# Optimization experiments

Measured on AMD Instinct MI355X. Metric: run time of the kernel, lower is better.

## Reference

```python
import jax, jax.numpy as jnp
import numpy as np

B, A, T = 256, 512, 21
DIM = 128
SC = 6
NHEAD, HD = 4, DIM // 4

def conv1d_relu(x, w, b, stride=2):
    # x: (N, C, L), w: (O, I, K)
    y = jax.lax.conv_general_dilated(x, w, (stride,), 'SAME', dimension_numbers=('NCH', 'OIH', 'NCH'))
    return jax.nn.relu(y + b[None, :, None])

def to_vector(feat, vm):
    vec_mask = vm[..., :-1] & vm[..., 1:]
    while vec_mask.ndim < feat.ndim:
        vec_mask = vec_mask[..., None]
    return jnp.where(vec_mask, feat[:, :, 1:] - feat[:, :, :-1], jnp.zeros_like(feat[:, :, 1:]))

def setup_inputs():
    key = jax.random.key(0)
    ks = jax.random.split(key, 24)
    f32 = jnp.float32
    inp = {}
    inp['position'] = jax.random.normal(ks[0], (B, A, T, 2), f32)
    inp['heading'] = jax.random.normal(ks[1], (B, A, T), f32)
    inp['velocity'] = jax.random.normal(ks[2], (B, A, T, 2), f32)
    inp['shape'] = jax.random.uniform(ks[3], (B, A, T, 2), f32)
    inp['current_state'] = jax.random.normal(ks[4], (B, SC), f32)
    inp['category'] = jax.random.randint(ks[5], (B, A), 0, 4)
    inp['valid_mask'] = jax.random.randint(ks[6], (B, A, T), 0, 2).astype(bool)
    # history encoder (CNN) params: 9 -> 32 -> 64 -> 128 channels, k=3, stride 2
    inp['conv1_w'] = jax.random.normal(ks[7], (32, 9, 3), f32) * 0.1
    inp['conv1_b'] = jnp.zeros((32,), f32)
    inp['conv2_w'] = jax.random.normal(ks[8], (64, 32, 3), f32) * 0.1
    inp['conv2_b'] = jnp.zeros((64,), f32)
    inp['conv3_w'] = jax.random.normal(ks[9], (128, 64, 3), f32) * 0.1
    inp['conv3_b'] = jnp.zeros((128,), f32)
    # StateAttentionEncoder params
    inp['se_w'] = jax.random.normal(ks[10], (SC, DIM), f32) * 0.02   # per-channel Linear(1,dim) weights
    inp['se_b'] = jnp.zeros((SC, DIM), f32)
    inp['pos_embed'] = jax.random.normal(ks[11], (1, SC, DIM), f32) * 0.02
    inp['query'] = jax.random.normal(ks[12], (1, 1, DIM), f32) * 0.02
    inp['in_proj_w'] = jax.random.normal(ks[13], (3 * DIM, DIM), f32) * (1.0 / np.sqrt(DIM))
    inp['in_proj_b'] = jnp.zeros((3 * DIM,), f32)
    inp['out_proj_w'] = jax.random.normal(ks[14], (DIM, DIM), f32) * (1.0 / np.sqrt(DIM))
    inp['out_proj_b'] = jnp.zeros((DIM,), f32)
    inp['type_emb'] = jax.random.normal(ks[15], (4, DIM), f32) * 0.02
    return inp

def reference(position, heading, velocity, shape, current_state, category, valid_mask,
              conv1_w, conv1_b, conv2_w, conv2_b, conv3_w, conv3_b,
              se_w, se_b, pos_embed, query, in_proj_w, in_proj_b, out_proj_w, out_proj_b,
              type_emb):
    # --- build per-step agent features (B, A, T-1, 9) ---
    heading_vec = to_vector(heading, valid_mask)
    valid_mask_vec = valid_mask[..., 1:] & valid_mask[..., :-1]
    agent_feature = jnp.concatenate([
        to_vector(position, valid_mask),
        to_vector(velocity, valid_mask),
        jnp.stack([jnp.cos(heading_vec), jnp.sin(heading_vec)], axis=-1),
        shape[:, :, 1:],
        valid_mask_vec.astype(jnp.float32)[..., None],
    ], axis=-1)
    bs, nA, Tm1, C = agent_feature.shape
    x = agent_feature.reshape(bs * nA, Tm1, C).transpose(0, 2, 1)  # (N, 9, T-1)
    # --- history CNN encoder (applied to all rows, then masked; same math as boolean gather/scatter) ---
    h = conv1d_relu(x, conv1_w, conv1_b)
    h = conv1d_relu(h, conv2_w, conv2_b)
    h = conv1d_relu(h, conv3_w, conv3_b)
    enc = h.mean(axis=-1)  # (N, DIM)
    valid_agent = valid_mask.any(-1).reshape(-1)
    x_agent = jnp.where(valid_agent[:, None], enc, 0.0).reshape(bs, nA, DIM)
    # --- ego state attention encoder (eval mode: no token dropout) ---
    ego = current_state[:, :SC]
    x_embed = ego[:, :, None] * se_w[None] + se_b[None] + pos_embed  # (B, SC, DIM)
    Wq, Wk, Wv = in_proj_w[:DIM], in_proj_w[DIM:2 * DIM], in_proj_w[2 * DIM:]
    bq, bk, bv = in_proj_b[:DIM], in_proj_b[DIM:2 * DIM], in_proj_b[2 * DIM:]
    q = (query[0, 0] @ Wq.T + bq).reshape(NHEAD, HD)             # (H, D)
    k = (x_embed @ Wk.T + bk).reshape(bs, SC, NHEAD, HD)          # (B, S, H, D)
    v = (x_embed @ Wv.T + bv).reshape(bs, SC, NHEAD, HD)
    scores = jnp.einsum('hd,bshd->bhs', q, k) * (1.0 / np.sqrt(HD))
    attn = jax.nn.softmax(scores, axis=-1)
    o = jnp.einsum('bhs,bshd->bhd', attn, v).reshape(bs, DIM)
    x_ego = o @ out_proj_w.T + out_proj_b                         # (B, DIM)
    x_agent = x_agent.at[:, 0].set(x_ego)
    # --- type embedding add ---
    return x_agent + type_emb[category]
```

## Files before the change

kernel.cpp:

```cpp
#include <hip/hip_runtime.h>
#include <hip/hip_bf16.h>


#define BB 256
#define AAG 512
#define TT 21
#define NAG (BB * AAG)

typedef __hip_bfloat16 bf16;
typedef __attribute__((ext_vector_type(8))) short s8v;
typedef __attribute__((ext_vector_type(4))) float f4v;

__device__ int g_dtype;
__device__ int g_mask_mode;
__device__ __align__(16) short g_w1p[32 * 64];
__device__ __align__(16) short g_w2p[64 * 96];
__device__ __align__(16) short g_w3p[128 * 192];
__device__ __align__(16) float g_b1[32];
__device__ __align__(16) float g_b2[64];
__device__ __align__(16) float g_b3[128];

template <int DT>
__device__ __forceinline__ float ldf(const void* p, long i) {
    if (DT) return __bfloat162float(((const bf16*)p)[i]);
    return ((const float*)p)[i];
}
template <int DT>
__device__ __forceinline__ void stf(void* p, long i, float v) {
    if (DT) ((bf16*)p)[i] = __float2bfloat16(v);
    else    ((float*)p)[i] = v;
}
__device__ __forceinline__ unsigned short f2bu(float x) {
    bf16 b = __float2bfloat16(x);
    union { bf16 b; unsigned short u; } cv; cv.b = b; return cv.u;
}
__device__ __forceinline__ float bu2f(unsigned short u) {
    union { unsigned int i; float f; } cv; cv.i = ((unsigned int)u) << 16; return cv.f;
}
template <int DT>
__device__ __forceinline__ float2 ldf2(const void* p, long i) {
    if (DT) {
        unsigned int u = *(const unsigned int*)((const bf16*)p + i);
        return make_float2(bu2f((unsigned short)(u & 0xffffu)),
                           bu2f((unsigned short)(u >> 16)));
    }
    return *(const float2*)((const float*)p + i);
}
__device__ __forceinline__ bool mask_at(const void* p, long i, int mode) {
    if (mode == 0) return ((const int*)p)[i] != 0;
    if (mode == 1) return ((const unsigned char*)p)[i] != 0;
    if (mode == 2) return ((const float*)p)[i] != 0.f;
    return (((const unsigned short*)p)[i] & 0x7fff) != 0;
}

__global__ void detect_kernel(const unsigned int* __restrict__ pw,
                              const unsigned char* __restrict__ m) {
    __shared__ int cls[4];
    __shared__ int mv;
    __shared__ int good;
    int tid = threadIdx.x;
    if (tid < 4) cls[tid] = 0;
    if (tid == 0) { mv = 0; good = 0; }
    __syncthreads();
    int g = 0;
    for (int i = tid; i < 1024; i += 256) {
        unsigned int w = pw[i];
        unsigned int h0 = w & 0xffffu, h1 = w >> 16;
        unsigned int e0 = (h0 >> 7) & 0xff, e1 = (h1 >> 7) & 0xff;
        if (h0 == 0 || (e0 >= 90 && e0 <= 160)) g++;
        if (h1 == 0 || (e1 >= 90 && e1 <= 160)) g++;
    }
    atomicAdd(&good, g);
    int l0 = 0, l1 = 0, l2 = 0, l3 = 0, lm = 0;
    for (int i = tid; i < 4096; i += 256) {
        int v = m[i];
        if (v) {
            switch (i & 3) { case 0: l0 = 1; break; case 1: l1 = 1; break;
                             case 2: l2 = 1; break; default: l3 = 1; }
            if (v > lm) lm = v;
        }
    }
    if (l0) atomicOr(&cls[0], 1);
    if (l1) atomicOr(&cls[1], 1);
    if (l2) atomicOr(&cls[2], 1);
    if (l3) atomicOr(&cls[3], 1);
    atomicMax(&mv, lm);
    __syncthreads();
    if (tid == 0) {
        g_dtype = (good >= 1740) ? 1 : 0;
        int mode;
        if (!cls[1] && !cls[2] && !cls[3]) mode = 0;
        else if (!cls[0] && !cls[1])       mode = 2;
        else if (mv <= 1)                  mode = 1;
        else                               mode = 3;
        g_mask_mode = mode;
    }
}

template <int DT>
__global__ void prep_weights_kernel(const void* __restrict__ w1, const void* __restrict__ b1,
                                    const void* __restrict__ w2, const void* __restrict__ b2,
                                    const void* __restrict__ w3, const void* __restrict__ b3) {
    if (g_dtype != DT) return;
    int tid = blockIdx.x * blockDim.x + threadIdx.x;
    int nt = gridDim.x * blockDim.x;
    for (int i = tid; i < 32 * 64; i += nt) {
        int oc = i >> 6, k = i & 63, tap = k >> 4, ic = k & 15;
        float v = (tap < 3 && ic < 9) ? ldf<DT>(w1, oc * 27 + ic * 3 + tap) : 0.f;
        g_w1p[i] = (short)f2bu(v);
    }
    for (int i = tid; i < 64 * 96; i += nt) {
        int oc = i / 96, k = i % 96, tap = k >> 5, ic = k & 31;
        g_w2p[i] = (short)f2bu(ldf<DT>(w2, oc * 96 + ic * 3 + tap));
    }
    for (int i = tid; i < 128 * 192; i += nt) {
        int oc = i / 192, k = i % 192, tap = k >> 6, ic = k & 63;
        g_w3p[i] = (short)f2bu(ldf<DT>(w3, oc * 192 + ic * 3 + tap));
    }
    for (int i = tid; i < 32; i += nt) g_b1[i] = ldf<DT>(b1, i);
    for (int i = tid; i < 64; i += nt) g_b2[i] = ldf<DT>(b2, i);
    for (int i = tid; i < 128; i += nt) g_b3[i] = ldf<DT>(b3, i);
}

#define FEAT_RS 24
#define FEAT_AS 568
#define H1_RS 40
#define H1_AS 440
#define H2_RS 72
#define H2_AS 504
#define C3_AS 392
#define OFF_H1 9088
#define OFF_VALID 32256
#define SMEM_BYTES 32320

#define MFMA16(a, b, c) __builtin_amdgcn_mfma_f32_16x16x32_bf16((a), (b), (c), 0, 0, 0)

template <int DT>
__global__ __launch_bounds__(256) void stage1_kernel(
    const void* __restrict__ pos, const void* __restrict__ heading,
    const void* __restrict__ vel, const void* __restrict__ shp,
    const void* __restrict__ vmask, const int* __restrict__ category,
    const void* __restrict__ type_emb, void* __restrict__ out) {
    if (g_dtype != DT) return;
    __shared__ __align__(16) char smem[SMEM_BYTES];
    short* feat = (short*)smem;
    short* h1   = (short*)smem + OFF_H1;
    short* h2   = (short*)smem;
    short* c3   = (short*)smem + OFF_H1;
    int* s_valid = (int*)(smem + OFF_VALID);

    const int tid = threadIdx.x;
    const int wave = tid >> 6, lane = tid & 63;
    const int col = lane & 15, quad = lane >> 4;
    const long agent0 = (long)blockIdx.x * 16;
    const int mode = g_mask_mode;

    if (tid < 16) s_valid[tid] = 0;
    {
        unsigned int* h1u = (unsigned int*)h1;
        h1u[(tid >> 4) * 220 + 200 + (tid & 15)] = 0;
    }
    __syncthreads();

    for (int idx = tid; idx < 16 * 22; idx += 256) {
        int ag = idx / 22, t = idx % 22;
        short* row = feat + ag * FEAT_AS + t * FEAT_RS;
        if (t >= 20) {
            *(uint4*)row = make_uint4(0, 0, 0, 0);
            *(uint4*)(row + 8) = make_uint4(0, 0, 0, 0);
            if (t == 20) {
                long base = (agent0 + ag) * TT + 20;
                if (mask_at(vmask, base, mode)) atomicOr(&s_valid[ag], 1);
            }
        } else {
            long base = (agent0 + ag) * TT + t;
            bool vmt = mask_at(vmask, base, mode);
            if (vmt) atomicOr(&s_valid[ag], 1);
            bool m2 = vmt && mask_at(vmask, base + 1, mode);
            float2 pa = ldf2<DT>(pos, base * 2), pb = ldf2<DT>(pos, base * 2 + 2);
            float2 va = ldf2<DT>(vel, base * 2), vb = ldf2<DT>(vel, base * 2 + 2);
            float hh0 = ldf<DT>(heading, base), hh1 = ldf<DT>(heading, base + 1);
            float2 sv = ldf2<DT>(shp, base * 2 + 2);
            float dh = m2 ? (hh1 - hh0) : 0.f;
            float sn, cn;
            __sincosf(dh, &sn, &cn);
            unsigned int p0 = f2bu(m2 ? pb.x - pa.x : 0.f) | ((unsigned int)f2bu(m2 ? pb.y - pa.y : 0.f) << 16);
            unsigned int p1 = f2bu(m2 ? vb.x - va.x : 0.f) | ((unsigned int)f2bu(m2 ? vb.y - va.y : 0.f) << 16);
            unsigned int p2 = f2bu(cn) | ((unsigned int)f2bu(sn) << 16);
            unsigned int p3 = f2bu(sv.x) | ((unsigned int)f2bu(sv.y) << 16);
            unsigned int p4 = (unsigned int)f2bu(m2 ? 1.f : 0.f);
            *(uint4*)row = make_uint4(p0, p1, p2, p3);
            *(uint4*)(row + 8) = make_uint4(p4, 0, 0, 0);
        }
    }
    __syncthreads();

    {
        int Mt = wave >> 1;
        int oc = Mt * 16 + col;
        s8v a0 = *(const s8v*)(g_w1p + oc * 64 + quad * 8);
        s8v a1 = *(const s8v*)(g_w1p + oc * 64 + 32 + quad * 8);
        int k0 = quad * 8, k1 = 32 + quad * 8;
        int tap0 = k0 >> 4, ic0 = k0 & 15;
        int tap1 = k1 >> 4, ic1 = k1 & 15;
        int ocr = Mt * 16 + quad * 4;
        f4v bia = *(const f4v*)(g_b1 + ocr);
        int ag = col;
        const short* agbase = feat + ag * FEAT_AS;
#pragma unroll
        for (int i = 0; i < 5; i++) {
            int p = (wave & 1) * 5 + i;
            const short* bb = agbase + 2 * p * FEAT_RS;
            s8v b0 = *(const s8v*)(bb + tap0 * FEAT_RS + ic0);
            s8v b1 = *(const s8v*)(bb + tap1 * FEAT_RS + ic1);
            f4v acc = {0.f, 0.f, 0.f, 0.f};
            acc = MFMA16(a0, b0, acc);
            acc = MFMA16(a1, b1, acc);
            unsigned int lo = f2bu(fmaxf(acc[0] + bia[0], 0.f)) | ((unsigned int)f2bu(fmaxf(acc[1] + bia[1], 0.f)) << 16);
            unsigned int hi = f2bu(fmaxf(acc[2] + bia[2], 0.f)) | ((unsigned int)f2bu(fmaxf(acc[3] + bia[3], 0.f)) << 16);
            *(uint2*)(h1 + ag * H1_AS + p * H1_RS + ocr) = make_uint2(lo, hi);
        }
    }
    __syncthreads();

    {
        unsigned int* h2u = (unsigned int*)h2;
        for (int i = tid; i < 1024; i += 256) {
            int a2 = i >> 6, r = (i >> 5) & 1, cc = i & 31;
            h2u[a2 * 252 + r * 216 + cc] = 0;
        }
        int Mt = wave;
        int oc = Mt * 16 + col;
        s8v a[3];
#pragma unroll
        for (int ks = 0; ks < 3; ks++)
            a[ks] = *(const s8v*)(g_w2p + oc * 96 + ks * 32 + quad * 8);
        int ocr = Mt * 16 + quad * 4;
        f4v bia = *(const f4v*)(g_b2 + ocr);
        int ag = col;
#pragma unroll
        for (int p = 0; p < 5; p++) {
            f4v acc = {0.f, 0.f, 0.f, 0.f};
#pragma unroll
            for (int ks = 0; ks < 3; ks++) {
                s8v b = *(const s8v*)(h1 + ag * H1_AS + (2 * p + ks) * H1_RS + quad * 8);
                acc = MFMA16(a[ks], b, acc);
            }
            unsigned int lo = f2bu(fmaxf(acc[0] + bia[0], 0.f)) | ((unsigned int)f2bu(fmaxf(acc[1] + bia[1], 0.f)) << 16);
            unsigned int hi = f2bu(fmaxf(acc[2] + bia[2], 0.f)) | ((unsigned int)f2bu(fmaxf(acc[3] + bia[3], 0.f)) << 16);
            *(uint2*)(h2 + ag * H2_AS + (p + 1) * H2_RS + ocr) = make_uint2(lo, hi);
        }
    }
    __syncthreads();

#pragma unroll
    for (int m2 = 0; m2 < 2; m2++) {
        int Mt = wave * 2 + m2;
        int oc = Mt * 16 + col;
        s8v a[6];
#pragma unroll
        for (int ks = 0; ks < 6; ks++)
            a[ks] = *(const s8v*)(g_w3p + oc * 192 + ks * 32 + quad * 8);
        int ocr = Mt * 16 + quad * 4;
        f4v bia = *(const f4v*)(g_b3 + ocr);
        int ag = col;
#pragma unroll
        for (int p = 0; p < 3; p++) {
            f4v acc = {0.f, 0.f, 0.f, 0.f};
#pragma unroll
            for (int ks = 0; ks < 6; ks++) {
                int kg = ks * 32 + quad * 8;
                int tap = kg >> 6, ic = kg & 63;
                s8v b = *(const s8v*)(h2 + ag * H2_AS + (2 * p + tap) * H2_RS + ic);
                acc = MFMA16(a[ks], b, acc);
            }
            unsigned int lo = f2bu(fmaxf(acc[0] + bia[0], 0.f)) | ((unsigned int)f2bu(fmaxf(acc[1] + bia[1], 0.f)) << 16);
            unsigned int hi = f2bu(fmaxf(acc[2] + bia[2], 0.f)) | ((unsigned int)f2bu(fmaxf(acc[3] + bia[3], 0.f)) << 16);
            *(uint2*)(c3 + ag * C3_AS + p * 128 + ocr) = make_uint2(lo, hi);
        }
    }
    __syncthreads();

    {
        int ag = tid >> 4;
        int ocg = (tid & 15) * 8;
        const short* cb = c3 + ag * C3_AS;
        s8v x0 = *(const s8v*)(cb + ocg);
        s8v x1 = *(const s8v*)(cb + 128 + ocg);
        s8v x2 = *(const s8v*)(cb + 256 + ocg);
        int valid = s_valid[ag];
        long agl = agent0 + ag;
        int cat = category[agl];
        float vals[8];
#pragma unroll
        for (int j = 0; j < 8; j++) {
            float m = (bu2f((unsigned short)x0[j]) + bu2f((unsigned short)x1[j]) +
                       bu2f((unsigned short)x2[j])) * (1.f / 3.f);
            vals[j] = valid ? m : 0.f;
        }
        if (DT) {
            s8v te = *(const s8v*)((const bf16*)type_emb + (long)cat * 128 + ocg);
            s8v o;
#pragma unroll
            for (int j = 0; j < 8; j++)
                o[j] = (short)f2bu(vals[j] + bu2f((unsigned short)te[j]));
            *(s8v*)((bf16*)out + agl * 128 + ocg) = o;
        } else {
            const float4* tep = (const float4*)((const float*)type_emb + (long)cat * 128 + ocg);
            float4 t0 = tep[0], t1 = tep[1];
            float4 o0 = make_float4(vals[0] + t0.x, vals[1] + t0.y, vals[2] + t0.z, vals[3] + t0.w);
            float4 o1 = make_float4(vals[4] + t1.x, vals[5] + t1.y, vals[6] + t1.z, vals[7] + t1.w);
            float4* op = (float4*)((float*)out + agl * 128 + ocg);
            op[0] = o0; op[1] = o1;
        }
    }
}

template <int DT>
__global__ __launch_bounds__(128) void stage2_kernel(
    const void* __restrict__ cs, const int* __restrict__ category,
    const void* __restrict__ se_w, const void* __restrict__ se_b,
    const void* __restrict__ pe, const void* __restrict__ query,
    const void* __restrict__ ipw, const void* __restrict__ ipb,
    const void* __restrict__ opw, const void* __restrict__ opb,
    const void* __restrict__ type_emb, void* __restrict__ out) {
    if (g_dtype != DT) return;
    int b = blockIdx.x, d = threadIdx.x;
    __shared__ float s_xe[6][128];
    __shared__ float s_qu[128];
    __shared__ float s_q[128];
    __shared__ float s_k[6][128];
    __shared__ float s_v[6][128];
    __shared__ float s_att[4][6];
    __shared__ float s_o[128];

    s_qu[d] = ldf<DT>(query, d);
#pragma unroll
    for (int s = 0; s < 6; s++) {
        float ego = ldf<DT>(cs, b * 6 + s);
        s_xe[s][d] = fmaf(ego, ldf<DT>(se_w, s * 128 + d),
                          ldf<DT>(se_b, s * 128 + d) + ldf<DT>(pe, s * 128 + d));
    }
    __syncthreads();

    float accq = ldf<DT>(ipb, d);
    float bk = ldf<DT>(ipb, 128 + d), bv = ldf<DT>(ipb, 256 + d);
    float acck[6], accv[6];
#pragma unroll
    for (int s = 0; s < 6; s++) { acck[s] = bk; accv[s] = bv; }
    for (int e = 0; e < 128; e++) {
        float wqe = ldf<DT>(ipw, (long)d * 128 + e);
        accq = fmaf(s_qu[e], wqe, accq);
        float wke = ldf<DT>(ipw, (long)(128 + d) * 128 + e);
        float wve = ldf<DT>(ipw, (long)(256 + d) * 128 + e);
#pragma unroll
        for (int s = 0; s < 6; s++) {
            float xe = s_xe[s][e];
            acck[s] = fmaf(xe, wke, acck[s]);
            accv[s] = fmaf(xe, wve, accv[s]);
        }
    }
    s_q[d] = accq;
#pragma unroll
    for (int s = 0; s < 6; s++) { s_k[s][d] = acck[s]; s_v[s][d] = accv[s]; }
    __syncthreads();

    if (d < 4) {
        float sc[6];
        float mx = -1e30f;
#pragma unroll
        for (int s = 0; s < 6; s++) {
            float t = 0.f;
            for (int q = 0; q < 32; q++) t = fmaf(s_q[d * 32 + q], s_k[s][d * 32 + q], t);
            t *= 0.17677669529663687f;
            sc[s] = t;
            mx = fmaxf(mx, t);
        }
        float sum = 0.f;
#pragma unroll
        for (int s = 0; s < 6; s++) { sc[s] = expf(sc[s] - mx); sum += sc[s]; }
        float inv = 1.f / sum;
#pragma unroll
        for (int s = 0; s < 6; s++) s_att[d][s] = sc[s] * inv;
    }
    __syncthreads();

    {
        int h = d >> 5;
        float o = 0.f;
#pragma unroll
        for (int s = 0; s < 6; s++) o = fmaf(s_att[h][s], s_v[s][d], o);
        s_o[d] = o;
    }
    __syncthreads();

    float acc = ldf<DT>(opb, d);
    for (int e = 0; e < 128; e++) acc = fmaf(s_o[e], ldf<DT>(opw, (long)d * 128 + e), acc);
    int cat = category[(long)b * AAG];
    stf<DT>(out, (long)b * AAG * 128 + d, acc + ldf<DT>(type_emb, cat * 128 + d));
}

extern "C" void kernel_launch(void* const* d_in, const int* in_sizes, int n_in,
                              void* d_out, int out_size, void* d_ws, size_t ws_size,
                              hipStream_t stream) {
    const void* position      = d_in[0];
    const void* heading       = d_in[1];
    const void* velocity      = d_in[2];
    const void* shape         = d_in[3];
    const void* current_state = d_in[4];
    const int*  category      = (const int*)d_in[5];
    const void* valid_mask    = d_in[6];
    const void* conv1_w = d_in[7];
    const void* conv1_b = d_in[8];
    const void* conv2_w = d_in[9];
    const void* conv2_b = d_in[10];
    const void* conv3_w = d_in[11];
    const void* conv3_b = d_in[12];
    const void* se_w    = d_in[13];
    const void* se_b    = d_in[14];
    const void* pos_embed = d_in[15];
    const void* query     = d_in[16];
    const void* in_proj_w = d_in[17];
    const void* in_proj_b = d_in[18];
    const void* out_proj_w = d_in[19];
    const void* out_proj_b = d_in[20];
    const void* type_emb   = d_in[21];

    hipLaunchKernelGGL(detect_kernel, dim3(1), dim3(256), 0, stream,
                       (const unsigned int*)position, (const unsigned char*)valid_mask);

    hipLaunchKernelGGL(prep_weights_kernel<0>, dim3(64), dim3(256), 0, stream,
                       conv1_w, conv1_b, conv2_w, conv2_b, conv3_w, conv3_b);
    hipLaunchKernelGGL(prep_weights_kernel<1>, dim3(64), dim3(256), 0, stream,
                       conv1_w, conv1_b, conv2_w, conv2_b, conv3_w, conv3_b);

    hipLaunchKernelGGL(stage1_kernel<0>, dim3(NAG / 16), dim3(256), 0, stream,
                       position, heading, velocity, shape, valid_mask, category, type_emb, d_out);
    hipLaunchKernelGGL(stage1_kernel<1>, dim3(NAG / 16), dim3(256), 0, stream,
                       position, heading, velocity, shape, valid_mask, category, type_emb, d_out);

    hipLaunchKernelGGL(stage2_kernel<0>, dim3(BB), dim3(128), 0, stream,
                       current_state, category, se_w, se_b, pos_embed, query,
                       in_proj_w, in_proj_b, out_proj_w, out_proj_b, type_emb, d_out);
    hipLaunchKernelGGL(stage2_kernel<1>, dim3(BB), dim3(128), 0, stream,
                       current_state, category, se_w, se_b, pos_embed, query,
                       in_proj_w, in_proj_b, out_proj_w, out_proj_b, type_emb, d_out);
}
```

Baseline: 304.5 us.

## Fuse launches into prep and combined kernels; fold query into key weights

Merges the dtype detection and weight-prep kernels into one prep kernel, which also precomputes the query projected through Wk (per-head vectors plus bias) so attention scores need only a dot with the embedded state. Stage1 and stage2 are fused into a single launch with a runtime dtype branch, replacing the separate launches per dtype. Stage2 applies attention before the V projection and splits the row dot products across 256 threads. Stage1 skips writing the agent-0 rows that stage2 overwrites, removing the write-write ordering dependence. Each block in the prep kernel redoes the detection scan, and the fused kernel carries code for both stages and both dtypes, which may raise register use.

```diff
diff --git a/kernel.cpp b/kernel.cpp
--- a/kernel.cpp
+++ b/kernel.cpp
@@ -19,6 +19,8 @@
 __device__ __align__(16) float g_b1[32];
 __device__ __align__(16) float g_b2[64];
 __device__ __align__(16) float g_b3[128];
+__device__ __align__(16) float g_wqk[4 * 128];
+__device__ __align__(16) float g_qb[4];
 
 template <int DT>
 __device__ __forceinline__ float ldf(const void* p, long i) {
@@ -53,11 +55,100 @@
     return (((const unsigned short*)p)[i] & 0x7fff) != 0;
 }
 
-__global__ void detect_kernel(const unsigned int* __restrict__ pw,
-                              const unsigned char* __restrict__ m) {
+template <int DT>
+__device__ __forceinline__ float rowdot64(const void* W, long off, const float* y) {
+    float acc = 0.f;
+    if (DT) {
+        const unsigned short* wr = (const unsigned short*)W + off;
+#pragma unroll
+        for (int i = 0; i < 8; i++) {
+            uint4 w = *(const uint4*)(wr + i * 8);
+            acc = fmaf(bu2f((unsigned short)(w.x & 0xffffu)), y[i * 8 + 0], acc);
+            acc = fmaf(bu2f((unsigned short)(w.x >> 16)),     y[i * 8 + 1], acc);
+            acc = fmaf(bu2f((unsigned short)(w.y & 0xffffu)), y[i * 8 + 2], acc);
+            acc = fmaf(bu2f((unsigned short)(w.y >> 16)),     y[i * 8 + 3], acc);
+            acc = fmaf(bu2f((unsigned short)(w.z & 0xffffu)), y[i * 8 + 4], acc);
+            acc = fmaf(bu2f((unsigned short)(w.z >> 16)),     y[i * 8 + 5], acc);
+            acc = fmaf(bu2f((unsigned short)(w.w & 0xffffu)), y[i * 8 + 6], acc);
+            acc = fmaf(bu2f((unsigned short)(w.w >> 16)),     y[i * 8 + 7], acc);
+        }
+    } else {
+        const float* wr = (const float*)W + off;
+#pragma unroll
+        for (int i = 0; i < 16; i++) {
+            float4 w = *(const float4*)(wr + i * 4);
+            acc = fmaf(w.x, y[i * 4 + 0], acc);
+            acc = fmaf(w.y, y[i * 4 + 1], acc);
+            acc = fmaf(w.z, y[i * 4 + 2], acc);
+            acc = fmaf(w.w, y[i * 4 + 3], acc);
+        }
+    }
+    return acc;
+}
+
+template <int DT>
+__device__ __forceinline__ void prep_body(const void* w1, const void* b1,
+                                          const void* w2, const void* b2,
+                                          const void* w3, const void* b3) {
+    int tid = blockIdx.x * 256 + threadIdx.x;
+    const int nt = 64 * 256;
+    for (int i = tid; i < 32 * 64; i += nt) {
+        int oc = i >> 6, k = i & 63, tap = k >> 4, ic = k & 15;
+        float v = (tap < 3 && ic < 9) ? ldf<DT>(w1, oc * 27 + ic * 3 + tap) : 0.f;
+        g_w1p[i] = (short)f2bu(v);
+    }
+    for (int i = tid; i < 64 * 96; i += nt) {
+        int oc = i / 96, k = i % 96, tap = k >> 5, ic = k & 31;
+        g_w2p[i] = (short)f2bu(ldf<DT>(w2, oc * 96 + ic * 3 + tap));
+    }
+    for (int i = tid; i < 128 * 192; i += nt) {
+        int oc = i / 192, k = i % 192, tap = k >> 6, ic = k & 63;
+        g_w3p[i] = (short)f2bu(ldf<DT>(w3, oc * 192 + ic * 3 + tap));
+    }
+    for (int i = tid; i < 32; i += nt) g_b1[i] = ldf<DT>(b1, i);
+    for (int i = tid; i < 64; i += nt) g_b2[i] = ldf<DT>(b2, i);
+    for (int i = tid; i < 128; i += nt) g_b3[i] = ldf<DT>(b3, i);
+}
+
+template <int DT>
+__device__ __forceinline__ void qprep_body(const void* query, const void* ipw,
+                                           const void* ipb, float* sq) {
+    int tid = threadIdx.x;
+    if (tid < 128) {
+        float acc = ldf<DT>(ipb, tid);
+        for (int e = 0; e < 128; e++)
+            acc = fmaf(ldf<DT>(query, e), ldf<DT>(ipw, (long)tid * 128 + e), acc);
+        sq[tid] = acc;
+    }
+    __syncthreads();
+    int e = tid & 127, hb = tid >> 7;
+    for (int h = hb; h < 4; h += 2) {
+        float acc = 0.f;
+#pragma unroll
+        for (int j = 0; j < 32; j++)
+            acc = fmaf(sq[h * 32 + j], ldf<DT>(ipw, (long)(128 + h * 32 + j) * 128 + e), acc);
+        g_wqk[h * 128 + e] = acc;
+    }
+    if (tid < 4) {
+        float acc = 0.f;
+#pragma unroll
+        for (int j = 0; j < 32; j++)
+            acc = fmaf(sq[tid * 32 + j], ldf<DT>(ipb, 128 + tid * 32 + j), acc);
+        g_qb[tid] = acc;
+    }
+}
+
+__global__ __launch_bounds__(256) void prep_kernel(
+    const unsigned int* __restrict__ pw, const unsigned char* __restrict__ m,
+    const void* __restrict__ w1, const void* __restrict__ b1,
+    const void* __restrict__ w2, const void* __restrict__ b2,
+    const void* __restrict__ w3, const void* __restrict__ b3,
+    const void* __restrict__ query, const void* __restrict__ ipw,
+    const void* __restrict__ ipb) {
     __shared__ int cls[4];
     __shared__ int mv;
     __shared__ int good;
+    __shared__ float sq[128];
     int tid = threadIdx.x;
     if (tid < 4) cls[tid] = 0;
     if (tid == 0) { mv = 0; good = 0; }
@@ -86,40 +177,21 @@
     if (l3) atomicOr(&cls[3], 1);
     atomicMax(&mv, lm);
     __syncthreads();
-    if (tid == 0) {
-        g_dtype = (good >= 1740) ? 1 : 0;
-        int mode;
-        if (!cls[1] && !cls[2] && !cls[3]) mode = 0;
-        else if (!cls[0] && !cls[1])       mode = 2;
-        else if (mv <= 1)                  mode = 1;
-        else                               mode = 3;
-        g_mask_mode = mode;
-    }
-}
-
-template <int DT>
-__global__ void prep_weights_kernel(const void* __restrict__ w1, const void* __restrict__ b1,
-                                    const void* __restrict__ w2, const void* __restrict__ b2,
-                                    const void* __restrict__ w3, const void* __restrict__ b3) {
-    if (g_dtype != DT) return;
-    int tid = blockIdx.x * blockDim.x + threadIdx.x;
-    int nt = gridDim.x * blockDim.x;
-    for (int i = tid; i < 32 * 64; i += nt) {
-        int oc = i >> 6, k = i & 63, tap = k >> 4, ic = k & 15;
-        float v = (tap < 3 && ic < 9) ? ldf<DT>(w1, oc * 27 + ic * 3 + tap) : 0.f;
-        g_w1p[i] = (short)f2bu(v);
-    }
-    for (int i = tid; i < 64 * 96; i += nt) {
-        int oc = i / 96, k = i % 96, tap = k >> 5, ic = k & 31;
-        g_w2p[i] = (short)f2bu(ldf<DT>(w2, oc * 96 + ic * 3 + tap));
-    }
-    for (int i = tid; i < 128 * 192; i += nt) {
-        int oc = i / 192, k = i % 192, tap = k >> 6, ic = k & 63;
-        g_w3p[i] = (short)f2bu(ldf<DT>(w3, oc * 192 + ic * 3 + tap));
-    }
-    for (int i = tid; i < 32; i += nt) g_b1[i] = ldf<DT>(b1, i);
-    for (int i = tid; i < 64; i += nt) g_b2[i] = ldf<DT>(b2, i);
-    for (int i = tid; i < 128; i += nt) g_b3[i] = ldf<DT>(b3, i);
+    int dt = (good >= 1740) ? 1 : 0;
+    int mode;
+    if (!cls[1] && !cls[2] && !cls[3]) mode = 0;
+    else if (!cls[0] && !cls[1])       mode = 2;
+    else if (mv <= 1)                  mode = 1;
+    else                               mode = 3;
+    if (blockIdx.x == 0 && tid == 0) { g_dtype = dt; g_mask_mode = mode; }
+
+    if (blockIdx.x < 64) {
+        if (dt) prep_body<1>(w1, b1, w2, b2, w3, b3);
+        else    prep_body<0>(w1, b1, w2, b2, w3, b3);
+    } else {
+        if (dt) qprep_body<1>(query, ipw, ipb, sq);
+        else    qprep_body<0>(query, ipw, ipb, sq);
+    }
 }
 
 #define FEAT_RS 24
@@ -136,13 +208,10 @@
 #define MFMA16(a, b, c) __builtin_amdgcn_mfma_f32_16x16x32_bf16((a), (b), (c), 0, 0, 0)
 
 template <int DT>
-__global__ __launch_bounds__(256) void stage1_kernel(
-    const void* __restrict__ pos, const void* __restrict__ heading,
-    const void* __restrict__ vel, const void* __restrict__ shp,
-    const void* __restrict__ vmask, const int* __restrict__ category,
-    const void* __restrict__ type_emb, void* __restrict__ out) {
-    if (g_dtype != DT) return;
-    __shared__ __align__(16) char smem[SMEM_BYTES];
+__device__ __forceinline__ void stage1_body(
+    const void* pos, const void* heading, const void* vel, const void* shp,
+    const void* vmask, const int* category, const void* type_emb, void* out,
+    char* smem, long agent0) {
     short* feat = (short*)smem;
     short* h1   = (short*)smem + OFF_H1;
     short* h2   = (short*)smem;
@@ -152,7 +221,6 @@
     const int tid = threadIdx.x;
     const int wave = tid >> 6, lane = tid & 63;
     const int col = lane & 15, quad = lane >> 4;
-    const long agent0 = (long)blockIdx.x * 16;
     const int mode = g_mask_mode;
 
     if (tid < 16) s_valid[tid] = 0;
@@ -290,6 +358,7 @@
         s8v x2 = *(const s8v*)(cb + 256 + ocg);
         int valid = s_valid[ag];
         long agl = agent0 + ag;
+        bool skip = ((agl & (AAG - 1)) == 0);
         int cat = category[agl];
         float vals[8];
 #pragma unroll
@@ -298,106 +367,126 @@
                        bu2f((unsigned short)x2[j])) * (1.f / 3.f);
             vals[j] = valid ? m : 0.f;
         }
-        if (DT) {
-            s8v te = *(const s8v*)((const bf16*)type_emb + (long)cat * 128 + ocg);
-            s8v o;
-#pragma unroll
-            for (int j = 0; j < 8; j++)
-                o[j] = (short)f2bu(vals[j] + bu2f((unsigned short)te[j]));
-            *(s8v*)((bf16*)out + agl * 128 + ocg) = o;
-        } else {
-            const float4* tep = (const float4*)((const float*)type_emb + (long)cat * 128 + ocg);
-            float4 t0 = tep[0], t1 = tep[1];
-            float4 o0 = make_float4(vals[0] + t0.x, vals[1] + t0.y, vals[2] + t0.z, vals[3] + t0.w);
-            float4 o1 = make_float4(vals[4] + t1.x, vals[5] + t1.y, vals[6] + t1.z, vals[7] + t1.w);
-            float4* op = (float4*)((float*)out + agl * 128 + ocg);
-            op[0] = o0; op[1] = o1;
-        }
-    }
-}
-
-template <int DT>
-__global__ __launch_bounds__(128) void stage2_kernel(
-    const void* __restrict__ cs, const int* __restrict__ category,
-    const void* __restrict__ se_w, const void* __restrict__ se_b,
-    const void* __restrict__ pe, const void* __restrict__ query,
-    const void* __restrict__ ipw, const void* __restrict__ ipb,
-    const void* __restrict__ opw, const void* __restrict__ opb,
-    const void* __restrict__ type_emb, void* __restrict__ out) {
-    if (g_dtype != DT) return;
-    int b = blockIdx.x, d = threadIdx.x;
-    __shared__ float s_xe[6][128];
-    __shared__ float s_qu[128];
-    __shared__ float s_q[128];
-    __shared__ float s_k[6][128];
-    __shared__ float s_v[6][128];
-    __shared__ float s_att[4][6];
-    __shared__ float s_o[128];
-
-    s_qu[d] = ldf<DT>(query, d);
-#pragma unroll
-    for (int s = 0; s < 6; s++) {
+        if (!skip) {
+            if (DT) {
+                s8v te = *(const s8v*)((const bf16*)type_emb + (long)cat * 128 + ocg);
+                s8v o;
+#pragma unroll
+                for (int j = 0; j < 8; j++)
+                    o[j] = (short)f2bu(vals[j] + bu2f((unsigned short)te[j]));
+                *(s8v*)((bf16*)out + agl * 128 + ocg) = o;
+            } else {
+                const float4* tep = (const float4*)((const float*)type_emb + (long)cat * 128 + ocg);
+                float4 t0 = tep[0], t1 = tep[1];
+                float4 o0 = make_float4(vals[0] + t0.x, vals[1] + t0.y, vals[2] + t0.z, vals[3] + t0.w);
+                float4 o1 = make_float4(vals[4] + t1.x, vals[5] + t1.y, vals[6] + t1.z, vals[7] + t1.w);
+                float4* op = (float4*)((float*)out + agl * 128 + ocg);
+                op[0] = o0; op[1] = o1;
+            }
+        }
+    }
+}
+
+template <int DT>
+__device__ __forceinline__ void stage2_body(
+    const void* cs, const int* category,
+    const void* se_w, const void* se_b, const void* pe,
+    const void* ipw, const void* ipb, const void* opw, const void* opb,
+    const void* type_emb, void* out, char* smem) {
+    const int b = blockIdx.x;
+    const int tid = threadIdx.x;
+    const int d = tid & 127, half = tid >> 7;
+
+    float* s_xe  = (float*)smem;
+    float* s_y   = s_xe + 768;
+    float* s_sc  = s_y + 512;
+    float* s_att = s_sc + 32;
+    float* s_o   = s_att + 32;
+    float* s_par = s_o + 128;
+
+    for (int idx = tid; idx < 768; idx += 256) {
+        int s = idx >> 7, dd = idx & 127;
         float ego = ldf<DT>(cs, b * 6 + s);
-        s_xe[s][d] = fmaf(ego, ldf<DT>(se_w, s * 128 + d),
-                          ldf<DT>(se_b, s * 128 + d) + ldf<DT>(pe, s * 128 + d));
-    }
-    __syncthreads();
-
-    float accq = ldf<DT>(ipb, d);
-    float bk = ldf<DT>(ipb, 128 + d), bv = ldf<DT>(ipb, 256 + d);
-    float acck[6], accv[6];
-#pragma unroll
-    for (int s = 0; s < 6; s++) { acck[s] = bk; accv[s] = bv; }
-    for (int e = 0; e < 128; e++) {
-        float wqe = ldf<DT>(ipw, (long)d * 128 + e);
-        accq = fmaf(s_qu[e], wqe, accq);
-        float wke = ldf<DT>(ipw, (long)(128 + d) * 128 + e);
-        float wve = ldf<DT>(ipw, (long)(256 + d) * 128 + e);
-#pragma unroll
-        for (int s = 0; s < 6; s++) {
-            float xe = s_xe[s][e];
-            acck[s] = fmaf(xe, wke, acck[s]);
-            accv[s] = fmaf(xe, wve, accv[s]);
-        }
-    }
-    s_q[d] = accq;
-#pragma unroll
-    for (int s = 0; s < 6; s++) { s_k[s][d] = acck[s]; s_v[s][d] = accv[s]; }
-    __syncthreads();
-
-    if (d < 4) {
-        float sc[6];
+        s_xe[idx] = fmaf(ego, ldf<DT>(se_w, s * 128 + dd),
+                         ldf<DT>(se_b, s * 128 + dd) + ldf<DT>(pe, s * 128 + dd));
+    }
+    __syncthreads();
+
+    if (tid < 96) {
+        int g = tid >> 2, lig = tid & 3;
+        int h = g / 6, s = g - h * 6;
+        const float* xr = s_xe + s * 128 + lig * 32;
+        const float* wr = g_wqk + h * 128 + lig * 32;
+        float t = 0.f;
+#pragma unroll
+        for (int e = 0; e < 32; e++) t = fmaf(xr[e], wr[e], t);
+        t += __shfl_xor(t, 1, 4);
+        t += __shfl_xor(t, 2, 4);
+        if (lig == 0) s_sc[g] = (t + g_qb[h]) * 0.17677669529663687f;
+    }
+    __syncthreads();
+
+    if (tid < 4) {
         float mx = -1e30f;
 #pragma unroll
-        for (int s = 0; s < 6; s++) {
-            float t = 0.f;
-            for (int q = 0; q < 32; q++) t = fmaf(s_q[d * 32 + q], s_k[s][d * 32 + q], t);
-            t *= 0.17677669529663687f;
-            sc[s] = t;
-            mx = fmaxf(mx, t);
-        }
-        float sum = 0.f;
-#pragma unroll
-        for (int s = 0; s < 6; s++) { sc[s] = expf(sc[s] - mx); sum += sc[s]; }
+        for (int s = 0; s < 6; s++) mx = fmaxf(mx, s_sc[tid * 6 + s]);
+        float sum = 0.f, ex[6];
+#pragma unroll
+        for (int s = 0; s < 6; s++) { ex[s] = expf(s_sc[tid * 6 + s] - mx); sum += ex[s]; }
         float inv = 1.f / sum;
 #pragma unroll
-        for (int s = 0; s < 6; s++) s_att[d][s] = sc[s] * inv;
+        for (int s = 0; s < 6; s++) s_att[tid * 6 + s] = ex[s] * inv;
+    }
+    __syncthreads();
+
+    for (int idx = tid; idx < 512; idx += 256) {
+        int h = idx >> 7, e = idx & 127;
+        float y = 0.f;
+#pragma unroll
+        for (int s = 0; s < 6; s++) y = fmaf(s_att[h * 6 + s], s_xe[s * 128 + e], y);
+        s_y[idx] = y;
     }
     __syncthreads();
 
     {
         int h = d >> 5;
-        float o = 0.f;
-#pragma unroll
-        for (int s = 0; s < 6; s++) o = fmaf(s_att[h][s], s_v[s][d], o);
-        s_o[d] = o;
-    }
-    __syncthreads();
-
-    float acc = ldf<DT>(opb, d);
-    for (int e = 0; e < 128; e++) acc = fmaf(s_o[e], ldf<DT>(opw, (long)d * 128 + e), acc);
-    int cat = category[(long)b * AAG];
-    stf<DT>(out, (long)b * AAG * 128 + d, acc + ldf<DT>(type_emb, cat * 128 + d));
+        const float* yr = s_y + h * 128 + half * 64;
+        s_par[half * 128 + d] = rowdot64<DT>(ipw, (long)(256 + d) * 128 + half * 64, yr);
+    }
+    __syncthreads();
+    if (half == 0) s_o[d] = s_par[d] + s_par[128 + d] + ldf<DT>(ipb, 256 + d);
+    __syncthreads();
+
+    {
+        const float* orr = s_o + half * 64;
+        s_par[half * 128 + d] = rowdot64<DT>(opw, (long)d * 128 + half * 64, orr);
+    }
+    __syncthreads();
+    if (half == 0) {
+        float x = s_par[d] + s_par[128 + d] + ldf<DT>(opb, d);
+        int cat = category[(long)b * AAG];
+        stf<DT>(out, (long)b * AAG * 128 + d, x + ldf<DT>(type_emb, cat * 128 + d));
+    }
+}
+
+__global__ __launch_bounds__(256) void fused_kernel(
+    const void* __restrict__ pos, const void* __restrict__ heading,
+    const void* __restrict__ vel, const void* __restrict__ shp,
+    const void* __restrict__ vmask, const int* __restrict__ category,
+    const void* __restrict__ type_emb, void* __restrict__ out,
+    const void* __restrict__ cs, const void* __restrict__ se_w,
+    const void* __restrict__ se_b, const void* __restrict__ pe,
+    const void* __restrict__ ipw, const void* __restrict__ ipb,
+    const void* __restrict__ opw, const void* __restrict__ opb) {
+    __shared__ __align__(16) char smem[SMEM_BYTES];
+    if (blockIdx.x < BB) {
+        if (g_dtype) stage2_body<1>(cs, category, se_w, se_b, pe, ipw, ipb, opw, opb, type_emb, out, smem);
+        else         stage2_body<0>(cs, category, se_w, se_b, pe, ipw, ipb, opw, opb, type_emb, out, smem);
+    } else {
+        long agent0 = (long)(blockIdx.x - BB) * 16;
+        if (g_dtype) stage1_body<1>(pos, heading, vel, shp, vmask, category, type_emb, out, smem, agent0);
+        else         stage1_body<0>(pos, heading, vel, shp, vmask, category, type_emb, out, smem, agent0);
+    }
 }
 
 extern "C" void kernel_launch(void* const* d_in, const int* in_sizes, int n_in,
@@ -426,23 +515,14 @@
     const void* out_proj_b = d_in[20];
     const void* type_emb   = d_in[21];
 
-    hipLaunchKernelGGL(detect_kernel, dim3(1), dim3(256), 0, stream,
-                       (const unsigned int*)position, (const unsigned char*)valid_mask);
-
-    hipLaunchKernelGGL(prep_weights_kernel<0>, dim3(64), dim3(256), 0, stream,
-                       conv1_w, conv1_b, conv2_w, conv2_b, conv3_w, conv3_b);
-    hipLaunchKernelGGL(prep_weights_kernel<1>, dim3(64), dim3(256), 0, stream,
-                       conv1_w, conv1_b, conv2_w, conv2_b, conv3_w, conv3_b);
-
-    hipLaunchKernelGGL(stage1_kernel<0>, dim3(NAG / 16), dim3(256), 0, stream,
-                       position, heading, velocity, shape, valid_mask, category, type_emb, d_out);
-    hipLaunchKernelGGL(stage1_kernel<1>, dim3(NAG / 16), dim3(256), 0, stream,
-                       position, heading, velocity, shape, valid_mask, category, type_emb, d_out);
-
-    hipLaunchKernelGGL(stage2_kernel<0>, dim3(BB), dim3(128), 0, stream,
-                       current_state, category, se_w, se_b, pos_embed, query,
-                       in_proj_w, in_proj_b, out_proj_w, out_proj_b, type_emb, d_out);
-    hipLaunchKernelGGL(stage2_kernel<1>, dim3(BB), dim3(128), 0, stream,
-                       current_state, category, se_w, se_b, pos_embed, query,
-                       in_proj_w, in_proj_b, out_proj_w, out_proj_b, type_emb, d_out);
-}
+    hipLaunchKernelGGL(prep_kernel, dim3(65), dim3(256), 0, stream,
+                       (const unsigned int*)position, (const unsigned char*)valid_mask,
+                       conv1_w, conv1_b, conv2_w, conv2_b, conv3_w, conv3_b,
+                       query, in_proj_w, in_proj_b);
+
+    hipLaunchKernelGGL(fused_kernel, dim3(BB + NAG / 16), dim3(256), 0, stream,
+                       position, heading, velocity, shape, valid_mask, category,
+                       type_emb, d_out,
+                       current_state, se_w, se_b, pos_embed,
+                       in_proj_w, in_proj_b, out_proj_w, out_proj_b);
+}
```

New measurement: 300.7 us. About the same (-1.2%).
